# Kernel tuning notes

Measured on AMD Instinct MI355X. Metric: run time of the kernel, lower is better.

## Reference

```python
import jax, jax.numpy as jnp
import numpy as np

QMIN, QMAX = -128.0, 127.0  # symmetric int8 (bit_width=8)

def setup_inputs() -> dict:
    key = jax.random.key(0)
    k1, k2, k3, k4, k5 = jax.random.split(key, 5)
    x = jax.random.normal(k1, (16, 4096, 1024), dtype=jnp.float32)
    weight_int = jax.random.randint(k2, (1024, 1024), 0, 127, dtype=jnp.int32)
    bias_int = jax.random.randint(k3, (1024,), 0, 127, dtype=jnp.int32)
    input_scale = jax.random.uniform(k4, (), dtype=jnp.float32, minval=0.01, maxval=1.0)
    output_scale = jax.random.uniform(k5, (), dtype=jnp.float32, minval=0.01, maxval=1.0)
    return {
        "x": x,
        "weight_int": weight_int,
        "bias_int": bias_int,
        "input_scale": input_scale,
        "output_scale": output_scale,
        "input_zero_point": 0,
        "output_zero_point": 0,
    }

def reference(x, weight_int, bias_int, input_scale, output_scale,
              input_zero_point, output_zero_point):
    # quantize input: round(x/scale)+zp, clamp to int8 range (kept in fp32,
    # matching x_int.float() in the original before the GEMM)
    x_q = jnp.clip(jnp.round(x / input_scale) + input_zero_point, QMIN, QMAX)
    # F.linear(x_q, W, b): [B,S,K] @ [N,K]^T + [N]
    out_int = jnp.einsum('bsk,nk->bsn', x_q, weight_int.astype(jnp.float32))
    out_int = out_int + bias_int.astype(jnp.float32)
    # dequantize output
    return (out_int - output_zero_point) * output_scale
```

## Files before the change

### kernel.cpp

```cpp
#include <hip/hip_runtime.h>
#include <stdint.h>

typedef int v4i __attribute__((ext_vector_type(4)));

#define AS1(p) ((const __attribute__((address_space(1))) void*)(p))
#define AS3(p) ((__attribute__((address_space(3))) void*)(p))

__global__ __launch_bounds__(256) void prep_kernel(
    const float* __restrict__ x, int8_t* __restrict__ xq,
    const int* __restrict__ w, int8_t* __restrict__ w8,
    const float* __restrict__ s_p, const int* __restrict__ izp_p)
{
    const int b = blockIdx.x;
    if (b >= 16384) {
        int t = (b - 16384) * 256 + threadIdx.x;
        int4 v = ((const int4*)w)[t];
        ((int*)w8)[t] = (v.x & 255) | ((v.y & 255) << 8) |
                        ((v.z & 255) << 16) | ((v.w & 255) << 24);
        return;
    }
    int t = b * 256 + threadIdx.x;
    float s = *s_p;
    float zp = (float)(*izp_p);
    const float4* xin = (const float4*)x + (size_t)t * 4;
    int words[4];
#pragma unroll
    for (int i = 0; i < 4; ++i) {
        float4 v = xin[i];
        float q0 = fminf(127.f, fmaxf(-128.f, rintf(v.x / s) + zp));
        float q1 = fminf(127.f, fmaxf(-128.f, rintf(v.y / s) + zp));
        float q2 = fminf(127.f, fmaxf(-128.f, rintf(v.z / s) + zp));
        float q3 = fminf(127.f, fmaxf(-128.f, rintf(v.w / s) + zp));
        words[i] = ((int)q0 & 255) | (((int)q1 & 255) << 8) |
                   (((int)q2 & 255) << 16) | (((int)q3 & 255) << 24);
    }
    ((int4*)xq)[t] = make_int4(words[0], words[1], words[2], words[3]);
}

#define GM 65536
#define GN 1024
#define GK 1024
#define NT 16

__global__ __launch_bounds__(256, 3) void gemm_i8_kernel(
    const int8_t* __restrict__ A,
    const int8_t* __restrict__ B,
    const int* __restrict__ bias,
    const float* __restrict__ osc_p, const int* __restrict__ ozp_p,
    float* __restrict__ out)
{
    __shared__ int8_t lds[3][2][8192];

    const int tid = threadIdx.x;
    const int w = tid >> 6, l = tid & 63;
    const int wr = w >> 1, wc = w & 1;
    const int r15 = l & 15, s4 = l >> 4;

    const int wg = blockIdx.x;
    const int lg = ((wg & 7) << 9) + (wg >> 3);
    const int bm0 = (lg >> 3) << 7;
    const int bn0 = (lg & 7) << 7;

    const int8_t* a_src[2];
    const int8_t* b_src[2];
    int st_dst[2];
#pragma unroll
    for (int e = 0; e < 2; ++e) {
        int o = e * 4096 + tid * 16;
        int row = o >> 6;
        int slot = (o >> 4) & 3;
        int gcol = ((slot ^ ((row >> 1) & 3)) << 4);
        a_src[e] = A + (size_t)(bm0 + row) * GK + gcol;
        b_src[e] = B + (size_t)(bn0 + row) * GK + gcol;
        st_dst[e] = e * 4096 + w * 1024;
    }

    int a_off[4], b_off[4];
#pragma unroll
    for (int i = 0; i < 4; ++i) {
        int row = wr * 64 + i * 16 + r15;
        a_off[i] = (row << 6) + ((s4 ^ ((row >> 1) & 3)) << 4);
    }
#pragma unroll
    for (int j = 0; j < 4; ++j) {
        int row = wc * 64 + j * 16 + r15;
        b_off[j] = (row << 6) + ((s4 ^ ((row >> 1) & 3)) << 4);
    }

    v4i acc[4][4];
#pragma unroll
    for (int i = 0; i < 4; ++i)
#pragma unroll
        for (int j = 0; j < 4; ++j) acc[i][j] = (v4i){0, 0, 0, 0};

#define STAGE(T, BUF) do { \
    __builtin_amdgcn_global_load_lds(AS1(a_src[0] + (T) * 64), AS3(&lds[BUF][0][st_dst[0]]), 16, 0, 0); \
    __builtin_amdgcn_global_load_lds(AS1(a_src[1] + (T) * 64), AS3(&lds[BUF][0][st_dst[1]]), 16, 0, 0); \
    __builtin_amdgcn_global_load_lds(AS1(b_src[0] + (T) * 64), AS3(&lds[BUF][1][st_dst[0]]), 16, 0, 0); \
    __builtin_amdgcn_global_load_lds(AS1(b_src[1] + (T) * 64), AS3(&lds[BUF][1][st_dst[1]]), 16, 0, 0); \
} while (0)

#define COMPUTE(BUF) do { \
    v4i af[4], bf[4]; \
    _Pragma("unroll") \
    for (int j = 0; j < 4; ++j) bf[j] = *(const v4i*)&lds[BUF][1][b_off[j]]; \
    _Pragma("unroll") \
    for (int i = 0; i < 4; ++i) af[i] = *(const v4i*)&lds[BUF][0][a_off[i]]; \
    __builtin_amdgcn_s_setprio(1); \
    _Pragma("unroll") \
    for (int i = 0; i < 4; ++i) \
    _Pragma("unroll") \
        for (int j = 0; j < 4; ++j) \
            acc[i][j] = __builtin_amdgcn_mfma_i32_16x16x64_i8(af[i], bf[j], acc[i][j], 0, 0, 0); \
    __builtin_amdgcn_s_setprio(0); \
} while (0)

    STAGE(0, 0);
    STAGE(1, 1);

    int c0 = 0, c1 = 1, c2 = 2;
#pragma unroll 1
    for (int t = 0; t < NT - 2; ++t) {
        asm volatile("s_waitcnt vmcnt(4)" ::: "memory");
        __builtin_amdgcn_s_barrier();
        STAGE(t + 2, c2);
        COMPUTE(c0);
        int tmp = c0; c0 = c1; c1 = c2; c2 = tmp;
    }
    asm volatile("s_waitcnt vmcnt(4)" ::: "memory");
    __builtin_amdgcn_s_barrier();
    COMPUTE(c0);
    asm volatile("s_waitcnt vmcnt(0)" ::: "memory");
    __builtin_amdgcn_s_barrier();
    COMPUTE(c1);

#undef STAGE
#undef COMPUTE

    const float osc = *osc_p;
    const int ozp = *ozp_p;
    int bj[4];
#pragma unroll
    for (int j = 0; j < 4; ++j)
        bj[j] = bias[bn0 + wc * 64 + j * 16 + r15] - ozp;

#pragma unroll
    for (int i = 0; i < 4; ++i) {
#pragma unroll
        for (int r = 0; r < 4; ++r) {
            const int mrow = bm0 + wr * 64 + i * 16 + s4 * 4 + r;
            float* op = out + (size_t)mrow * GN + bn0 + wc * 64 + r15;
#pragma unroll
            for (int j = 0; j < 4; ++j)
                op[j * 16] = (float)(acc[i][j][r] + bj[j]) * osc;
        }
    }
}

extern "C" void kernel_launch(void* const* d_in, const int* in_sizes, int n_in,
                              void* d_out, int out_size, void* d_ws, size_t ws_size,
                              hipStream_t stream)
{
    const float* x         = (const float*)d_in[0];
    const int*   w_int     = (const int*)d_in[1];
    const int*   b_int     = (const int*)d_in[2];
    const float* in_scale  = (const float*)d_in[3];
    const float* out_scale = (const float*)d_in[4];
    const int*   izp       = (const int*)d_in[5];
    const int*   ozp       = (const int*)d_in[6];
    float* out = (float*)d_out;

    int8_t* xq = (int8_t*)d_ws;
    int8_t* w8 = (int8_t*)d_ws + (size_t)64 * 1024 * 1024;

    prep_kernel<<<16384 + 1024, 256, 0, stream>>>(x, xq, w_int, w8, in_scale, izp);
    gemm_i8_kernel<<<4096, 256, 0, stream>>>(xq, w8, b_int, out_scale, ozp, out);
}
```

Baseline: 195.5 us.

## Load GEMM operands directly from global memory into registers, drop LDS pipeline

Removes the triple-buffered LDS staging through global_load_lds, its barriers and waitcnts. Each wave now loads its MFMA fragments straight from global memory into registers in a fully unrolled K loop and relies on cache reuse between waves. Output stores also become nontemporal with a reordered loop. The change avoids LDS traffic and barrier syncs, but each fragment is now fetched once per wave that uses it, and the row-strided 16-byte loads may coalesce poorly and expose global latency.

New measurement: 294.3 us. 1.5x slower.

```diff
diff --git a/kernel.cpp b/kernel.cpp
--- a/kernel.cpp
+++ b/kernel.cpp
@@ -2,9 +2,6 @@
 #include <stdint.h>
 
 typedef int v4i __attribute__((ext_vector_type(4)));
-
-#define AS1(p) ((const __attribute__((address_space(1))) void*)(p))
-#define AS3(p) ((__attribute__((address_space(3))) void*)(p))
 
 __global__ __launch_bounds__(256) void prep_kernel(
     const float* __restrict__ x, int8_t* __restrict__ xq,
@@ -49,8 +46,6 @@
     const float* __restrict__ osc_p, const int* __restrict__ ozp_p,
     float* __restrict__ out)
 {
-    __shared__ int8_t lds[3][2][8192];
-
     const int tid = threadIdx.x;
     const int w = tid >> 6, l = tid & 63;
     const int wr = w >> 1, wc = w & 1;
@@ -61,31 +56,14 @@
     const int bm0 = (lg >> 3) << 7;
     const int bn0 = (lg & 7) << 7;
 
-    const int8_t* a_src[2];
-    const int8_t* b_src[2];
-    int st_dst[2];
+    const int8_t* ap[4];
+    const int8_t* bp[4];
 #pragma unroll
-    for (int e = 0; e < 2; ++e) {
-        int o = e * 4096 + tid * 16;
-        int row = o >> 6;
-        int slot = (o >> 4) & 3;
-        int gcol = ((slot ^ ((row >> 1) & 3)) << 4);
-        a_src[e] = A + (size_t)(bm0 + row) * GK + gcol;
-        b_src[e] = B + (size_t)(bn0 + row) * GK + gcol;
-        st_dst[e] = e * 4096 + w * 1024;
-    }
-
-    int a_off[4], b_off[4];
+    for (int i = 0; i < 4; ++i)
+        ap[i] = A + (size_t)(bm0 + wr * 64 + i * 16 + r15) * GK + s4 * 16;
 #pragma unroll
-    for (int i = 0; i < 4; ++i) {
-        int row = wr * 64 + i * 16 + r15;
-        a_off[i] = (row << 6) + ((s4 ^ ((row >> 1) & 3)) << 4);
-    }
-#pragma unroll
-    for (int j = 0; j < 4; ++j) {
-        int row = wc * 64 + j * 16 + r15;
-        b_off[j] = (row << 6) + ((s4 ^ ((row >> 1) & 3)) << 4);
-    }
+    for (int j = 0; j < 4; ++j)
+        bp[j] = B + (size_t)(bn0 + wc * 64 + j * 16 + r15) * GK + s4 * 16;
 
     v4i acc[4][4];
 #pragma unroll
@@ -93,49 +71,21 @@
 #pragma unroll
         for (int j = 0; j < 4; ++j) acc[i][j] = (v4i){0, 0, 0, 0};
 
-#define STAGE(T, BUF) do { \
-    __builtin_amdgcn_global_load_lds(AS1(a_src[0] + (T) * 64), AS3(&lds[BUF][0][st_dst[0]]), 16, 0, 0); \
-    __builtin_amdgcn_global_load_lds(AS1(a_src[1] + (T) * 64), AS3(&lds[BUF][0][st_dst[1]]), 16, 0, 0); \
-    __builtin_amdgcn_global_load_lds(AS1(b_src[0] + (T) * 64), AS3(&lds[BUF][1][st_dst[0]]), 16, 0, 0); \
-    __builtin_amdgcn_global_load_lds(AS1(b_src[1] + (T) * 64), AS3(&lds[BUF][1][st_dst[1]]), 16, 0, 0); \
-} while (0)
-
-#define COMPUTE(BUF) do { \
-    v4i af[4], bf[4]; \
-    _Pragma("unroll") \
-    for (int j = 0; j < 4; ++j) bf[j] = *(const v4i*)&lds[BUF][1][b_off[j]]; \
-    _Pragma("unroll") \
-    for (int i = 0; i < 4; ++i) af[i] = *(const v4i*)&lds[BUF][0][a_off[i]]; \
-    __builtin_amdgcn_s_setprio(1); \
-    _Pragma("unroll") \
-    for (int i = 0; i < 4; ++i) \
-    _Pragma("unroll") \
-        for (int j = 0; j < 4; ++j) \
-            acc[i][j] = __builtin_amdgcn_mfma_i32_16x16x64_i8(af[i], bf[j], acc[i][j], 0, 0, 0); \
-    __builtin_amdgcn_s_setprio(0); \
-} while (0)
-
-    STAGE(0, 0);
-    STAGE(1, 1);
-
-    int c0 = 0, c1 = 1, c2 = 2;
-#pragma unroll 1
-    for (int t = 0; t < NT - 2; ++t) {
-        asm volatile("s_waitcnt vmcnt(4)" ::: "memory");
-        __builtin_amdgcn_s_barrier();
-        STAGE(t + 2, c2);
-        COMPUTE(c0);
-        int tmp = c0; c0 = c1; c1 = c2; c2 = tmp;
+#pragma unroll
+    for (int t = 0; t < NT; ++t) {
+        v4i af[4], bf[4];
+#pragma unroll
+        for (int i = 0; i < 4; ++i) af[i] = *(const v4i*)(ap[i] + t * 64);
+#pragma unroll
+        for (int j = 0; j < 4; ++j) bf[j] = *(const v4i*)(bp[j] + t * 64);
+        __builtin_amdgcn_s_setprio(1);
+#pragma unroll
+        for (int i = 0; i < 4; ++i)
+#pragma unroll
+            for (int j = 0; j < 4; ++j)
+                acc[i][j] = __builtin_amdgcn_mfma_i32_16x16x64_i8(af[i], bf[j], acc[i][j], 0, 0, 0);
+        __builtin_amdgcn_s_setprio(0);
     }
-    asm volatile("s_waitcnt vmcnt(4)" ::: "memory");
-    __builtin_amdgcn_s_barrier();
-    COMPUTE(c0);
-    asm volatile("s_waitcnt vmcnt(0)" ::: "memory");
-    __builtin_amdgcn_s_barrier();
-    COMPUTE(c1);
-
-#undef STAGE
-#undef COMPUTE
 
     const float osc = *osc_p;
     const int ozp = *ozp_p;
@@ -146,13 +96,15 @@
 
 #pragma unroll
     for (int i = 0; i < 4; ++i) {
+        const int mrow = bm0 + wr * 64 + i * 16 + s4 * 4;
 #pragma unroll
-        for (int r = 0; r < 4; ++r) {
-            const int mrow = bm0 + wr * 64 + i * 16 + s4 * 4 + r;
-            float* op = out + (size_t)mrow * GN + bn0 + wc * 64 + r15;
+        for (int j = 0; j < 4; ++j) {
+            const int n = bn0 + wc * 64 + j * 16 + r15;
+            float* op = out + (size_t)mrow * GN + n;
 #pragma unroll
-            for (int j = 0; j < 4; ++j)
-                op[j * 16] = (float)(acc[i][j][r] + bj[j]) * osc;
+            for (int r = 0; r < 4; ++r)
+                __builtin_nontemporal_store((float)(acc[i][j][r] + bj[j]) * osc,
+                                            op + (size_t)r * GN);
         }
     }
 }
```
